# Kernel tuning notes

Hardware: AMD Instinct MI355X
Metric: run time of the kernel (lower is better)

## Reference

```python
import jax, jax.numpy as jnp
import numpy as np

H = 4096
NUM_HEADS = 32
D = 128
SEQ_LEN = 1024
CTX = 4096


def setup_inputs() -> dict:
    key = jax.random.key(0)
    k1, k2, k3, k4 = jax.random.split(key, 4)
    X = jax.random.normal(k1, (SEQ_LEN, H), dtype=jnp.float32)
    # Linear weight [out=3H, in=H]; scale ~1/sqrt(H) so attention logits are O(1)
    W = jax.random.normal(k2, (3 * H, H), dtype=jnp.float32) * (1.0 / np.sqrt(H))
    cache_K = jax.random.normal(k3, (1, CTX, NUM_HEADS, D), dtype=jnp.float32)
    cache_V = jax.random.normal(k4, (1, CTX, NUM_HEADS, D), dtype=jnp.float32)
    return {"X": X, "W": W, "cache_K": cache_K, "cache_V": cache_V}


def reference(X, W, cache_K, cache_V):
    seq_len, h = X.shape
    nh, d = cache_K.shape[2], cache_K.shape[3]
    # fused QKV projection (Linear, no bias): X @ W^T -> [seq_len, 3H]
    qkv = X @ W.T
    q, k, v = jnp.split(qkv, 3, axis=1)
    q = q.reshape(1, seq_len, nh, d)
    k = k.reshape(1, seq_len, nh, d)
    v = v.reshape(1, seq_len, nh, d)
    # concat KV cache along the sequence dim (cache_K[:, :P] with P = full cache)
    k_full = jnp.concatenate([cache_K, k], axis=1)  # [1, ctx+seq, nh, d]
    v_full = jnp.concatenate([cache_V, v], axis=1)
    scale = 1.0 / np.sqrt(d)
    # scores: [1, nh, seq_q, kv_len]
    scores = jnp.einsum("bqhd,bkhd->bhqk", q, k_full) * scale
    weights = jax.nn.softmax(scores, axis=-1)
    out = jnp.einsum("bhqk,bkhd->bqhd", weights, v_full)  # [1, seq, nh, d]
    return out.reshape(seq_len, h)
```

## Files before the change

### kernel.cpp

```cpp
#include <hip/hip_runtime.h>
#include <hip/hip_bf16.h>
#include <stdint.h>

#define H_DIM 4096
#define NH 32
#define HD 128
#define SEQ 1024
#define CTX 4096
#define KVL (CTX + SEQ)
#define W3H (3 * H_DIM)
#define ATTN_SCALE 0.08838834764831845f

typedef short short8 __attribute__((ext_vector_type(8)));
typedef float f32x4 __attribute__((ext_vector_type(4)));

#define GLOAD_LDS16(g, l)                                             \
  __builtin_amdgcn_global_load_lds(                                   \
      (const __attribute__((address_space(1))) void*)(g),             \
      (__attribute__((address_space(3))) void*)(l), 16, 0, 0)

__device__ __forceinline__ unsigned short f2b(float f) {
  union { float f; unsigned u; } v; v.f = f;
  return (unsigned short)((v.u + 0x7FFFu + ((v.u >> 16) & 1u)) >> 16);
}
__device__ __forceinline__ float b2f(unsigned short u) {
  union { unsigned u; float f; } v; v.u = ((unsigned)u) << 16;
  return v.f;
}

__global__ void k_cvt2(const float* __restrict__ X, const float* __restrict__ W,
                       unsigned short* __restrict__ Xb, unsigned short* __restrict__ Wb) {
  const int nx = SEQ * H_DIM / 4;
  const int nw = W3H * H_DIM / 4;
  int i = blockIdx.x * 256 + threadIdx.x;
  const float* s;
  unsigned short* d;
  int j;
  if (i < nx) { s = X; d = Xb; j = i; }
  else { j = i - nx; if (j >= nw) return; s = W; d = Wb; }
  float4 v = reinterpret_cast<const float4*>(s)[j];
  ushort4 o;
  o.x = f2b(v.x); o.y = f2b(v.y); o.z = f2b(v.z); o.w = f2b(v.w);
  reinterpret_cast<ushort4*>(d)[j] = o;
}

#define GBM 256
#define GBN 192
#define GBK 64
#define GNKT (H_DIM / GBK)
#define LBUF 57344
__global__ __launch_bounds__(512, 1) void k_gemm_qkv(
    const unsigned short* __restrict__ A,
    const unsigned short* __restrict__ B,
    unsigned short* __restrict__ C) {
  __shared__ __align__(16) char Lds[2 * LBUF];
  const int tid = threadIdx.x;
  const int lane = tid & 63;
  const int wid = tid >> 6;
  const int wm = wid >> 2;
  const int wn = wid & 3;
  const int lq = lane >> 4;
  const int lr = lane & 15;

  const int id = blockIdx.x;
  const int wg = (id & 7) * 32 + (id >> 3);
  const int bm = wg & 3;
  const int bn = wg >> 2;

  const unsigned short* Abase = A + (size_t)(bm * GBM) * H_DIM;
  const unsigned short* Bbase = B + (size_t)(bn * GBN) * H_DIM;
  const int sel = 8 * ((lane & 7) ^ (lane >> 3));
  const int srow = lane >> 3;

#define GA2(t, j0, b)                                                          \
  {                                                                            \
    _Pragma("unroll") for (int j = (j0); j < (j0) + 2; ++j) {                  \
      int c = wid + j * 8;                                                     \
      GLOAD_LDS16(Abase + (size_t)(c * 8 + srow) * H_DIM + (t) * GBK + sel,    \
                  Lds + (b) * LBUF + c * 1024);                                \
    }                                                                          \
  }
#define GB2(t, j0, b)                                                          \
  {                                                                            \
    _Pragma("unroll") for (int j = (j0); j < (j0) + 2; ++j) {                  \
      int c = wid + j * 8;                                                     \
      GLOAD_LDS16(Bbase + (size_t)(c * 8 + srow) * H_DIM + (t) * GBK + sel,    \
                  Lds + (b) * LBUF + 32768 + c * 1024);                        \
    }                                                                          \
  }
#define GB1(t, j0, b)                                                          \
  {                                                                            \
    int c = wid + (j0) * 8;                                                    \
    GLOAD_LDS16(Bbase + (size_t)(c * 8 + srow) * H_DIM + (t) * GBK + sel,      \
                Lds + (b) * LBUF + 32768 + c * 1024);                          \
  }

  f32x4 acc[8][3] = {};

#define GPHASE(T, q)                                                           \
  {                                                                            \
    const int cb_ = ((T) & 1) * LBUF;                                          \
    short8 af[2][2];                                                           \
    _Pragma("unroll") for (int mm = 0; mm < 2; ++mm)                           \
      _Pragma("unroll") for (int kk = 0; kk < 2; ++kk)                         \
        af[mm][kk] = *reinterpret_cast<const short8*>(                         \
            Lds + cb_ + (wm * 128 + ((q) * 2 + mm) * 16 + lr) * 128 +          \
            16 * ((kk * 4 + lq) ^ (lr & 7)));                                  \
    if ((q) == 0) {                                                            \
      _Pragma("unroll") for (int n = 0; n < 3; ++n)                            \
        _Pragma("unroll") for (int kk = 0; kk < 2; ++kk)                       \
          bfr[n][kk] = *reinterpret_cast<const short8*>(                       \
              Lds + cb_ + 32768 + (wn * 48 + n * 16 + lr) * 128 +              \
              16 * ((kk * 4 + lq) ^ (lr & 7)));                                \
    }                                                                          \
    if ((q) == 0 && (T) + 1 < GNKT) GA2((T) + 1, 0, ((T) + 1) & 1);            \
    if ((q) == 1 && (T) + 1 < GNKT) GA2((T) + 1, 2, ((T) + 1) & 1);            \
    if ((q) == 2 && (T) + 2 < GNKT) GB2((T) + 2, 0, (T) & 1);                  \
    if ((q) == 3 && (T) + 2 < GNKT) GB1((T) + 2, 2, (T) & 1);                  \
    if ((q) == 3) {                                                            \
      if ((T) + 2 < GNKT) {                                                    \
        asm volatile("s_waitcnt vmcnt(3)" ::: "memory");                       \
      } else {                                                                 \
        asm volatile("s_waitcnt vmcnt(0)" ::: "memory");                       \
      }                                                                        \
    }                                                                          \
    __builtin_amdgcn_sched_barrier(0);                                         \
    __builtin_amdgcn_s_barrier();                                              \
    asm volatile("s_waitcnt lgkmcnt(0)" ::: "memory");                         \
    __builtin_amdgcn_sched_barrier(0);                                         \
    __builtin_amdgcn_s_setprio(1);                                             \
    _Pragma("unroll") for (int kk = 0; kk < 2; ++kk)                           \
      _Pragma("unroll") for (int mm = 0; mm < 2; ++mm)                         \
        _Pragma("unroll") for (int n = 0; n < 3; ++n)                          \
          acc[(q) * 2 + mm][n] = __builtin_amdgcn_mfma_f32_16x16x32_bf16(      \
              af[mm][kk], bfr[n][kk], acc[(q) * 2 + mm][n], 0, 0, 0);          \
    __builtin_amdgcn_s_setprio(0);                                             \
    __builtin_amdgcn_sched_barrier(0);                                         \
    __builtin_amdgcn_s_barrier();                                              \
    __builtin_amdgcn_sched_barrier(0);                                         \
  }

  GA2(0, 0, 0);
  GA2(0, 2, 0);
  GB2(0, 0, 0);
  GB1(0, 2, 0);
  GB2(1, 0, 1);
  GB1(1, 2, 1);
  asm volatile("s_waitcnt vmcnt(3)" ::: "memory");
  __builtin_amdgcn_sched_barrier(0);
  __builtin_amdgcn_s_barrier();
  __builtin_amdgcn_sched_barrier(0);

  for (int T = 0; T < GNKT; ++T) {
    short8 bfr[3][2];
    GPHASE(T, 0);
    GPHASE(T, 1);
    GPHASE(T, 2);
    GPHASE(T, 3);
  }

  const int r0 = bm * GBM + wm * 128 + lq * 4;
  const int c0 = bn * GBN + wn * 48 + lr;
#pragma unroll
  for (int m = 0; m < 8; ++m)
#pragma unroll
    for (int n = 0; n < 3; ++n)
#pragma unroll
      for (int r = 0; r < 4; ++r)
        C[(size_t)(r0 + m * 16 + r) * W3H + c0 + n * 16] = f2b(acc[m][n][r]);
#undef GA2
#undef GB2
#undef GB1
#undef GPHASE
}

__global__ void k_build_k(const float* __restrict__ cK, const unsigned short* __restrict__ QKV,
                          unsigned short* __restrict__ Kb) {
  int idx = (blockIdx.x * 256 + threadIdx.x) * 4;
  if (idx >= NH * KVL * HD) return;
  int h = idx / (KVL * HD);
  int rem = idx % (KVL * HD);
  int kv = rem / HD;
  int d = rem % HD;
  ushort4 o;
  if (kv < CTX) {
    float4 v = *reinterpret_cast<const float4*>(cK + ((size_t)kv * NH + h) * HD + d);
    o.x = f2b(v.x); o.y = f2b(v.y); o.z = f2b(v.z); o.w = f2b(v.w);
  } else {
    o = *reinterpret_cast<const ushort4*>(QKV + (size_t)(kv - CTX) * W3H + H_DIM + h * HD + d);
  }
  *reinterpret_cast<ushort4*>(Kb + idx) = o;
}

__global__ void k_build_vt(const float* __restrict__ cV, const unsigned short* __restrict__ QKV,
                           unsigned short* __restrict__ Vt) {
  __shared__ unsigned short T[HD][66];
  const int h = blockIdx.y;
  const int kt = blockIdx.x;
  const int t = threadIdx.x;
#pragma unroll
  for (int e = 0; e < 8; ++e) {
    int idx = (t + e * 256) * 4;
    int kvl = idx >> 7;
    int d = idx & 127;
    int kv = kt * 64 + kvl;
    unsigned short a, b, c, w;
    if (kv < CTX) {
      float4 v = *reinterpret_cast<const float4*>(cV + ((size_t)kv * NH + h) * HD + d);
      a = f2b(v.x); b = f2b(v.y); c = f2b(v.z); w = f2b(v.w);
    } else {
      ushort4 u = *reinterpret_cast<const ushort4*>(QKV + (size_t)(kv - CTX) * W3H + 2 * H_DIM + h * HD + d);
      a = u.x; b = u.y; c = u.z; w = u.w;
    }
    T[d][kvl] = a; T[d + 1][kvl] = b; T[d + 2][kvl] = c; T[d + 3][kvl] = w;
  }
  __syncthreads();
#pragma unroll
  for (int e = 0; e < 8; ++e) {
    int idx = (t + e * 256) * 4;
    int d = idx >> 6;
    int kv0 = idx & 63;
    ushort4 o;
    o.x = T[d][kv0]; o.y = T[d][kv0 + 1]; o.z = T[d][kv0 + 2]; o.w = T[d][kv0 + 3];
    *reinterpret_cast<ushort4*>(Vt + ((size_t)h * HD + d) * KVL + kt * 64 + kv0) = o;
  }
}

#define KVT 64
#define NT (KVL / KVT)
#define NT2 (NT / 2)
__global__ __launch_bounds__(256, 2) void k_attn(
    const unsigned short* __restrict__ QKV,
    const unsigned short* __restrict__ Kb,
    const unsigned short* __restrict__ Vt,
    float* __restrict__ A0,
    float* __restrict__ A1,
    float* __restrict__ Mp,
    float* __restrict__ Lp) {
  __shared__ unsigned short Ks[2][KVT * HD];
  __shared__ unsigned short Vs[2][KVT * HD];
  const int tid = threadIdx.x, lane = tid & 63, wid = tid >> 6;
  const int g = lane >> 4;
  const int qi = lane & 15;
  const int id = blockIdx.x;
  const int xcd = id & 7, slot = id >> 3;
  const int h = xcd * 4 + (slot >> 4);
  const int rem = slot & 15;
  const int qt = rem >> 1;
  const int split = rem & 1;
  const int kt0 = split * NT2;
  const int q0 = qt * 128 + wid * 32;

  short8 qf[2][4];
#pragma unroll
  for (int hf = 0; hf < 2; ++hf)
#pragma unroll
    for (int c = 0; c < 4; ++c) {
      short8 q = *reinterpret_cast<const short8*>(
          QKV + (size_t)(q0 + hf * 16 + qi) * W3H + h * HD + c * 32 + g * 8);
      short8 t;
#pragma unroll
      for (int j = 0; j < 8; ++j) t[j] = (short)f2b(b2f((unsigned short)q[j]) * ATTN_SCALE);
      qf[hf][c] = t;
    }

  float m_r[2] = {-1e30f, -1e30f}, l_r[2] = {0.f, 0.f};
  f32x4 acc_o[2][8] = {};

  const char* Kh = (const char*)(Kb + (size_t)h * KVL * HD);
  const char* Vh = (const char*)(Vt + (size_t)h * HD * KVL);

#define STAGE_K(t, b)                                                          \
  {                                                                            \
    _Pragma("unroll") for (int i = 0; i < 4; ++i) {                            \
      int c = wid * 4 + i;                                                     \
      int krow = c * 4 + (lane >> 4);                                          \
      int klcb = (16 * (lane & 15)) ^ ((krow & 7) << 4);                       \
      GLOAD_LDS16(Kh + (size_t)((t) * KVT + krow) * 256 + klcb,                \
                  (char*)Ks[b] + c * 1024);                                    \
    }                                                                          \
  }
#define STAGE_V(t, b)                                                          \
  {                                                                            \
    _Pragma("unroll") for (int i = 0; i < 4; ++i) {                            \
      int c = wid * 4 + i;                                                     \
      int vrow = c * 8 + (lane >> 3);                                          \
      int vlcb = (16 * (lane & 7)) ^ ((vrow & 7) << 4);                        \
      GLOAD_LDS16(Vh + (size_t)vrow * (KVL * 2) + (size_t)(t) * 128 + vlcb,    \
                  (char*)Vs[b] + c * 1024);                                    \
    }                                                                          \
  }
#define QKT(buf, S)                                                            \
  {                                                                            \
    _Pragma("unroll") for (int n = 0; n < 4; ++n) {                            \
      S[0][n] = (f32x4){0.f, 0.f, 0.f, 0.f};                                   \
      S[1][n] = (f32x4){0.f, 0.f, 0.f, 0.f};                                   \
    }                                                                          \
    __builtin_amdgcn_s_setprio(1);                                             \
    _Pragma("unroll") for (int n = 0; n < 4; ++n) {                            \
      int row = n * 16 + qi;                                                   \
      _Pragma("unroll") for (int c = 0; c < 4; ++c) {                          \
        int cb = (c * 32 + g * 8) * 2;                                         \
        short8 kf = *reinterpret_cast<const short8*>(                          \
            (const char*)Ks[buf] + row * 256 + (cb ^ ((row & 7) << 4)));       \
        S[0][n] = __builtin_amdgcn_mfma_f32_16x16x32_bf16(kf, qf[0][c], S[0][n], 0, 0, 0); \
        S[1][n] = __builtin_amdgcn_mfma_f32_16x16x32_bf16(kf, qf[1][c], S[1][n], 0, 0, 0); \
      }                                                                        \
    }                                                                          \
    __builtin_amdgcn_s_setprio(0);                                             \
  }

  const int i0 = ((2 * (g & 1) + 0) * 16 + qi) * 4;
  const int i1 = ((2 * (g & 1) + 1) * 16 + qi) * 4;

#define SMPV(S, vb)                                                            \
  {                                                                            \
    float p[2][4][4];                                                          \
    int okv = 1;                                                               \
    float tmax[2];                                                             \
    _Pragma("unroll") for (int hf = 0; hf < 2; ++hf) {                         \
      float t0 = S[hf][0][0];                                                  \
      _Pragma("unroll") for (int n = 0; n < 4; ++n)                            \
        _Pragma("unroll") for (int r = 0; r < 4; ++r)                          \
          t0 = fmaxf(t0, S[hf][n][r]);                                         \
      t0 = fmaxf(t0, __shfl_xor(t0, 16, 64));                                  \
      t0 = fmaxf(t0, __shfl_xor(t0, 32, 64));                                  \
      tmax[hf] = t0;                                                           \
      okv &= (t0 <= m_r[hf] + 8.0f);                                           \
    }                                                                          \
    if (!__all(okv)) {                                                         \
      _Pragma("unroll") for (int hf = 0; hf < 2; ++hf) {                       \
        float mn = fmaxf(m_r[hf], tmax[hf]);                                   \
        float alpha = __expf(m_r[hf] - mn);                                    \
        l_r[hf] *= alpha;                                                      \
        m_r[hf] = mn;                                                          \
        _Pragma("unroll") for (int nd = 0; nd < 8; ++nd) acc_o[hf][nd] *= alpha; \
      }                                                                        \
    }                                                                          \
    _Pragma("unroll") for (int hf = 0; hf < 2; ++hf) {                         \
      float sum = 0.f;                                                         \
      _Pragma("unroll") for (int n = 0; n < 4; ++n)                            \
        _Pragma("unroll") for (int r = 0; r < 4; ++r) {                        \
          p[hf][n][r] = __expf(S[hf][n][r] - m_r[hf]);                         \
          sum += p[hf][n][r];                                                  \
        }                                                                      \
      sum += __shfl_xor(sum, 16, 64);                                          \
      sum += __shfl_xor(sum, 32, 64);                                          \
      l_r[hf] += sum;                                                          \
    }                                                                          \
    unsigned pr[2][4][2];                                                      \
    _Pragma("unroll") for (int hf = 0; hf < 2; ++hf)                           \
      _Pragma("unroll") for (int n = 0; n < 4; ++n)                            \
        _Pragma("unroll") for (int rr = 0; rr < 2; ++rr) {                     \
          union { __hip_bfloat162 b; unsigned u; } cv;                         \
          cv.b = __float22bfloat162_rn(                                        \
              make_float2(p[hf][n][2 * rr], p[hf][n][2 * rr + 1]));            \
          pr[hf][n][rr] = cv.u;                                                \
        }                                                                      \
    _Pragma("unroll") for (int kc = 0; kc < 2; ++kc) {                         \
      short8 pv[2];                                                            \
      _Pragma("unroll") for (int hf = 0; hf < 2; ++hf) {                       \
        int a0 = __builtin_amdgcn_ds_bpermute(i0, (int)pr[hf][2 * kc][0]);     \
        int b0 = __builtin_amdgcn_ds_bpermute(i0, (int)pr[hf][2 * kc + 1][0]); \
        int a1 = __builtin_amdgcn_ds_bpermute(i0, (int)pr[hf][2 * kc][1]);     \
        int b1 = __builtin_amdgcn_ds_bpermute(i0, (int)pr[hf][2 * kc + 1][1]); \
        int a2 = __builtin_amdgcn_ds_bpermute(i1, (int)pr[hf][2 * kc][0]);     \
        int b2 = __builtin_amdgcn_ds_bpermute(i1, (int)pr[hf][2 * kc + 1][0]); \
        int a3 = __builtin_amdgcn_ds_bpermute(i1, (int)pr[hf][2 * kc][1]);     \
        int b3 = __builtin_amdgcn_ds_bpermute(i1, (int)pr[hf][2 * kc + 1][1]); \
        union { int i[4]; short8 s8; } u;                                      \
        u.i[0] = (g < 2) ? a0 : b0;                                            \
        u.i[1] = (g < 2) ? a1 : b1;                                            \
        u.i[2] = (g < 2) ? a2 : b2;                                            \
        u.i[3] = (g < 2) ? a3 : b3;                                            \
        pv[hf] = u.s8;                                                         \
      }                                                                        \
      __builtin_amdgcn_s_setprio(1);                                           \
      _Pragma("unroll") for (int nd = 0; nd < 8; ++nd) {                       \
        int row = nd * 16 + qi;                                                \
        int cb = kc * 64 + g * 16;                                             \
        short8 vf = *reinterpret_cast<const short8*>(                          \
            (const char*)Vs[vb] + row * 128 + (cb ^ ((row & 7) << 4)));        \
        acc_o[0][nd] = __builtin_amdgcn_mfma_f32_16x16x32_bf16(vf, pv[0], acc_o[0][nd], 0, 0, 0); \
        acc_o[1][nd] = __builtin_amdgcn_mfma_f32_16x16x32_bf16(vf, pv[1], acc_o[1][nd], 0, 0, 0); \
      }                                                                        \
      __builtin_amdgcn_s_setprio(0);                                           \
    }                                                                          \
  }

#define BODY(t, SC, SN)                                                        \
  {                                                                            \
    const int cur = (t) & 1;                                                   \
    if ((t) + 2 < NT2) STAGE_K(kt0 + (t) + 2, cur);                            \
    if ((t) + 1 < NT2) QKT(cur ^ 1, SN);                                       \
    SMPV(SC, cur);                                                             \
    __syncthreads();                                                           \
    if ((t) + 2 < NT2) STAGE_V(kt0 + (t) + 2, cur);                            \
  }

  STAGE_K(kt0, 0);
  STAGE_V(kt0, 0);
  STAGE_K(kt0 + 1, 1);
  STAGE_V(kt0 + 1, 1);
  __syncthreads();

  f32x4 sA[2][4], sB[2][4];
  QKT(0, sA);

  for (int tt = 0; tt < NT2; tt += 2) {
    BODY(tt, sA, sB);
    BODY(tt + 1, sB, sA);
  }

  float* Op = split ? A1 : A0;
#pragma unroll
  for (int hf = 0; hf < 2; ++hf) {
    float* orow = Op + (size_t)(q0 + hf * 16 + qi) * H_DIM + h * HD;
#pragma unroll
    for (int nd = 0; nd < 8; ++nd)
      *reinterpret_cast<float4*>(orow + nd * 16 + g * 4) =
          *reinterpret_cast<const float4*>(&acc_o[hf][nd]);
    if (g == 0) {
      int q = q0 + hf * 16 + qi;
      Mp[split * (NH * SEQ) + h * SEQ + q] = m_r[hf];
      Lp[split * (NH * SEQ) + h * SEQ + q] = l_r[hf];
    }
  }
#undef STAGE_K
#undef STAGE_V
#undef QKT
#undef SMPV
#undef BODY
}

__global__ void k_combine(const float* __restrict__ A1, const float* __restrict__ Mp,
                          const float* __restrict__ Lp, float* __restrict__ out) {
  int i4 = blockIdx.x * 256 + threadIdx.x;
  int q = i4 >> 10;
  int c4 = i4 & 1023;
  int h = c4 >> 5;
  float m0 = Mp[h * SEQ + q], m1 = Mp[NH * SEQ + h * SEQ + q];
  float l0 = Lp[h * SEQ + q], l1 = Lp[NH * SEQ + h * SEQ + q];
  float M = fmaxf(m0, m1);
  float w0 = __expf(m0 - M), w1 = __expf(m1 - M);
  float inv = 1.0f / (w0 * l0 + w1 * l1);
  float4 a0 = reinterpret_cast<const float4*>(out)[i4];
  float4 a1 = reinterpret_cast<const float4*>(A1)[i4];
  float4 o;
  o.x = (w0 * a0.x + w1 * a1.x) * inv;
  o.y = (w0 * a0.y + w1 * a1.y) * inv;
  o.z = (w0 * a0.z + w1 * a1.z) * inv;
  o.w = (w0 * a0.w + w1 * a1.w) * inv;
  reinterpret_cast<float4*>(out)[i4] = o;
}

extern "C" void kernel_launch(void* const* d_in, const int* in_sizes, int n_in,
                              void* d_out, int out_size, void* d_ws, size_t ws_size,
                              hipStream_t stream) {
  const float* X = (const float*)d_in[0];
  const float* W = (const float*)d_in[1];
  const float* cK = (const float*)d_in[2];
  const float* cV = (const float*)d_in[3];
  float* out = (float*)d_out;
  char* ws = (char*)d_ws;

  unsigned short* Xb = (unsigned short*)(ws);
  float* Mp = (float*)(ws);
  float* Lp = (float*)(ws + (256 << 10));
  unsigned short* QKVb = (unsigned short*)(ws + ((size_t)8 << 20));
  unsigned short* Wb = (unsigned short*)(ws + ((size_t)32 << 20));
  unsigned short* Kb = (unsigned short*)(ws + ((size_t)32 << 20));
  unsigned short* Vt = (unsigned short*)(ws + ((size_t)72 << 20));
  float* A1 = (float*)(ws + ((size_t)112 << 20));

  int ncvt = (SEQ * H_DIM + W3H * H_DIM) / 4;
  k_cvt2<<<(ncvt + 255) / 256, 256, 0, stream>>>(X, W, Xb, Wb);

  k_gemm_qkv<<<(SEQ / GBM) * (W3H / GBN), 512, 0, stream>>>(Xb, Wb, QKVb);

  k_build_k<<<(NH * KVL * HD / 4) / 256, 256, 0, stream>>>(cK, QKVb, Kb);
  dim3 gv(KVL / 64, NH);
  k_build_vt<<<gv, 256, 0, stream>>>(cV, QKVb, Vt);

  k_attn<<<SEQ / 128 * NH * 2, 256, 0, stream>>>(QKVb, Kb, Vt, out, A1, Mp, Lp);
  k_combine<<<(SEQ * H_DIM / 4) / 256, 256, 0, stream>>>(A1, Mp, Lp, out);
}
```

Baseline: 323.1 us.

## Permute K rows to drop P bpermutes, use exp2 with folded log2e, defer row-sum reduction

Loads K tile rows in a permuted order so the QK^T MFMA output layout directly matches the B-operand layout for the PV MFMA, removing the ds_bpermute shuffles. Folds log2(e) into the Q scale and uses raw v_exp_f32 (exp2) instead of __expf. The per-tile cross-lane sum reduction for l is moved to a single reduction after the loop. These cut per-tile LDS permute traffic and ALU work, but the permutation must stay consistent with the V layout for correctness.

```diff
diff --git a/kernel.cpp b/kernel.cpp
--- a/kernel.cpp
+++ b/kernel.cpp
@@ -9,7 +9,7 @@
 #define CTX 4096
 #define KVL (CTX + SEQ)
 #define W3H (3 * H_DIM)
-#define ATTN_SCALE 0.08838834764831845f
+#define QK_SCALE_LOG2E 0.12751743075305723f
 
 typedef short short8 __attribute__((ext_vector_type(8)));
 typedef float f32x4 __attribute__((ext_vector_type(4)));
@@ -26,6 +26,11 @@
 __device__ __forceinline__ float b2f(unsigned short u) {
   union { unsigned u; float f; } v; v.u = ((unsigned)u) << 16;
   return v.f;
+}
+__device__ __forceinline__ float fexp2(float x) {
+  float r;
+  asm("v_exp_f32 %0, %1" : "=v"(r) : "v"(x));
+  return r;
 }
 
 __global__ void k_cvt2(const float* __restrict__ X, const float* __restrict__ W,
@@ -226,6 +231,7 @@
   }
 }
 
+#define PKV(x) ((((x) & 32)) | (((x) & 12) << 1) | (((x) & 16) >> 2) | ((x) & 3))
 #define KVT 64
 #define NT (KVL / KVT)
 #define NT2 (NT / 2)
@@ -260,7 +266,7 @@
           QKV + (size_t)(q0 + hf * 16 + qi) * W3H + h * HD + c * 32 + g * 8);
       short8 t;
 #pragma unroll
-      for (int j = 0; j < 8; ++j) t[j] = (short)f2b(b2f((unsigned short)q[j]) * ATTN_SCALE);
+      for (int j = 0; j < 8; ++j) t[j] = (short)f2b(b2f((unsigned short)q[j]) * QK_SCALE_LOG2E);
       qf[hf][c] = t;
     }
 
@@ -274,9 +280,10 @@
   {                                                                            \
     _Pragma("unroll") for (int i = 0; i < 4; ++i) {                            \
       int c = wid * 4 + i;                                                     \
-      int krow = c * 4 + (lane >> 4);                                          \
+      int krow = c * 4 + (lane >> 4);                             \
+      int kglob = PKV(krow);                       \
       int klcb = (16 * (lane & 15)) ^ ((krow & 7) << 4);                       \
-      GLOAD_LDS16(Kh + (size_t)((t) * KVT + krow) * 256 + klcb,                \
+      GLOAD_LDS16(Kh + (size_t)((t) * KVT + kglob) * 256 + klcb,               \
                   (char*)Ks[b] + c * 1024);                                    \
     }                                                                          \
   }
@@ -309,9 +316,6 @@
     }                                                                          \
     __builtin_amdgcn_s_setprio(0);                                             \
   }
-
-  const int i0 = ((2 * (g & 1) + 0) * 16 + qi) * 4;
-  const int i1 = ((2 * (g & 1) + 1) * 16 + qi) * 4;
 
 #define SMPV(S, vb)                                                            \
   {                                                                            \
@@ -331,7 +335,7 @@
     if (!__all(okv)) {                                                         \
       _Pragma("unroll") for (int hf = 0; hf < 2; ++hf) {                       \
         float mn = fmaxf(m_r[hf], tmax[hf]);                                   \
-        float alpha = __expf(m_r[hf] - mn);                                    \
+        float alpha = fexp2(m_r[hf] - mn);                                     \
         l_r[hf] *= alpha;                                                      \
         m_r[hf] = mn;                                                          \
         _Pragma("unroll") for (int nd = 0; nd < 8; ++nd) acc_o[hf][nd] *= alpha; \
@@ -341,12 +345,10 @@
       float sum = 0.f;                                                         \
       _Pragma("unroll") for (int n = 0; n < 4; ++n)                            \
         _Pragma("unroll") for (int r = 0; r < 4; ++r) {                        \
-          p[hf][n][r] = __expf(S[hf][n][r] - m_r[hf]);                         \
+          p[hf][n][r] = fexp2(S[hf][n][r] - m_r[hf]);                          \
           sum += p[hf][n][r];                                                  \
         }                                                                      \
-      sum += __shfl_xor(sum, 16, 64);                                          \
-      sum += __shfl_xor(sum, 32, 64);                                          \
-      l_r[hf] += sum;                                                          \
+      l_r[hf] += sum;     \
     }                                                                          \
     unsigned pr[2][4][2];                                                      \
     _Pragma("unroll") for (int hf = 0; hf < 2; ++hf)                           \
@@ -360,19 +362,11 @@
     _Pragma("unroll") for (int kc = 0; kc < 2; ++kc) {                         \
       short8 pv[2];                                                            \
       _Pragma("unroll") for (int hf = 0; hf < 2; ++hf) {                       \
-        int a0 = __builtin_amdgcn_ds_bpermute(i0, (int)pr[hf][2 * kc][0]);     \
-        int b0 = __builtin_amdgcn_ds_bpermute(i0, (int)pr[hf][2 * kc + 1][0]); \
-        int a1 = __builtin_amdgcn_ds_bpermute(i0, (int)pr[hf][2 * kc][1]);     \
-        int b1 = __builtin_amdgcn_ds_bpermute(i0, (int)pr[hf][2 * kc + 1][1]); \
-        int a2 = __builtin_amdgcn_ds_bpermute(i1, (int)pr[hf][2 * kc][0]);     \
-        int b2 = __builtin_amdgcn_ds_bpermute(i1, (int)pr[hf][2 * kc + 1][0]); \
-        int a3 = __builtin_amdgcn_ds_bpermute(i1, (int)pr[hf][2 * kc][1]);     \
-        int b3 = __builtin_amdgcn_ds_bpermute(i1, (int)pr[hf][2 * kc + 1][1]); \
-        union { int i[4]; short8 s8; } u;                                      \
-        u.i[0] = (g < 2) ? a0 : b0;                                            \
-        u.i[1] = (g < 2) ? a1 : b1;                                            \
-        u.i[2] = (g < 2) ? a2 : b2;                                            \
-        u.i[3] = (g < 2) ? a3 : b3;                                            \
+        union { unsigned u[4]; short8 s8; } u;                                 \
+        u.u[0] = pr[hf][2 * kc][0];                                            \
+        u.u[1] = pr[hf][2 * kc][1];                                            \
+        u.u[2] = pr[hf][2 * kc + 1][0];                                        \
+        u.u[3] = pr[hf][2 * kc + 1][1];                                        \
         pv[hf] = u.s8;                                                         \
       }                                                                        \
       __builtin_amdgcn_s_setprio(1);                                           \
@@ -412,6 +406,12 @@
     BODY(tt + 1, sB, sA);
   }
 
+#pragma unroll
+  for (int hf = 0; hf < 2; ++hf) {
+    l_r[hf] += __shfl_xor(l_r[hf], 16, 64);
+    l_r[hf] += __shfl_xor(l_r[hf], 32, 64);
+  }
+
   float* Op = split ? A1 : A0;
 #pragma unroll
   for (int hf = 0; hf < 2; ++hf) {
@@ -442,7 +442,7 @@
   float m0 = Mp[h * SEQ + q], m1 = Mp[NH * SEQ + h * SEQ + q];
   float l0 = Lp[h * SEQ + q], l1 = Lp[NH * SEQ + h * SEQ + q];
   float M = fmaxf(m0, m1);
-  float w0 = __expf(m0 - M), w1 = __expf(m1 - M);
+  float w0 = fexp2(m0 - M), w1 = fexp2(m1 - M);
   float inv = 1.0f / (w0 * l0 + w1 * l1);
   float4 a0 = reinterpret_cast<const float4*>(out)[i4];
   float4 a1 = reinterpret_cast<const float4*>(A1)[i4];
```

Measured after the change: 360.0 us. 11.4% more time.
